# Kernel tuning notes

Hardware: AMD Instinct MI355X
Metric: run time of the kernel (lower is better)

## Reference

```python
import jax, jax.numpy as jnp
import numpy as np

N, E, H = 50000, 800000, 128
LN_EPS = 1e-5  # torch nn.LayerNorm default


def layer_norm(x, gamma, beta):
    mu = jnp.mean(x, axis=-1, keepdims=True)
    var = jnp.mean((x - mu) ** 2, axis=-1, keepdims=True)
    return (x - mu) * jax.lax.rsqrt(var + LN_EPS) * gamma + beta


def setup_inputs() -> dict:
    key = jax.random.key(0)
    ks = jax.random.split(key, 8)
    sc = 1.0 / np.sqrt(2 * H)
    return {
        "x": jax.random.normal(ks[0], (N, H), dtype=jnp.float32),
        "edge_index": jax.random.randint(ks[1], (2, E), 0, N, dtype=jnp.int64),
        "edge_weights": jax.random.uniform(ks[2], (E,), dtype=jnp.float32),
        "msg_w": jax.random.normal(ks[3], (2 * H, H), dtype=jnp.float32) * sc,
        "msg_b": jnp.zeros((H,), jnp.float32),
        "msg_g": jnp.ones((H,), jnp.float32),
        "msg_beta": jnp.zeros((H,), jnp.float32),
        "upd_w": jax.random.normal(ks[4], (2 * H, H), dtype=jnp.float32) * sc,
        "upd_b": jnp.zeros((H,), jnp.float32),
        "upd_g": jnp.ones((H,), jnp.float32),
        "upd_beta": jnp.zeros((H,), jnp.float32),
        "gate_w": jax.random.normal(ks[5], (H, 1), dtype=jnp.float32) / np.sqrt(H),
        "gate_b": jnp.zeros((1,), jnp.float32),
    }


def reference(x, edge_index, edge_weights, msg_w, msg_b, msg_g, msg_beta,
              upd_w, upd_b, upd_g, upd_beta, gate_w, gate_b):
    num_nodes = x.shape[0]
    src, dst = edge_index[0], edge_index[1]
    # per-edge gather -> MLP -> weighted message  [E, H]
    em = jnp.concatenate([x[src], x[dst]], axis=-1)          # [E, 2H]
    em = jax.nn.relu(layer_norm(em @ msg_w + msg_b, msg_g, msg_beta))
    em = em * edge_weights[:, None]
    # scatter-add to destination nodes + mean normalization
    msgs = jax.ops.segment_sum(em, dst, num_segments=num_nodes)           # [N, H]
    counts = jax.ops.segment_sum(jnp.ones((src.shape[0], 1), x.dtype), dst,
                                 num_segments=num_nodes)                  # [N, 1]
    valid = (counts > 0).astype(x.dtype)
    messages = msgs / (counts + 1e-8) * valid
    # gated update
    gate = jax.nn.sigmoid(x @ gate_w + gate_b)                            # [N, 1]
    combined = jnp.concatenate([x, messages], axis=-1)                    # [N, 2H]
    h_new = jax.nn.relu(layer_norm(combined @ upd_w + upd_b, upd_g, upd_beta))
    return gate * h_new + (1.0 - gate) * x
```

## Files before the change

### kernel.cpp

```cpp
#include <hip/hip_runtime.h>
#include <math.h>

#define H 128
#define LN_EPS 1e-5f

typedef __attribute__((ext_vector_type(8))) short  bf16x8;
typedef __attribute__((ext_vector_type(4))) float  f32x4;
typedef __attribute__((ext_vector_type(8))) unsigned short ushort8v;

__device__ __forceinline__ int imin(int a, int b) { return a < b ? a : b; }
__device__ __forceinline__ int clampi(int v, int lo, int hi) { return v < lo ? lo : (v > hi ? hi : v); }
__device__ __forceinline__ unsigned short f2bf(float f) {
    unsigned u = __float_as_uint(f);
    unsigned r = (u + 0x7fffu + ((u >> 16) & 1u)) >> 16;
    return (unsigned short)r;
}
__device__ __forceinline__ float bf2f(unsigned short u) {
    return __uint_as_float(((unsigned)u) << 16);
}

__global__ void count_kernel(const int* __restrict__ dst, int* __restrict__ cnt, int E, int n) {
    int i = blockIdx.x * blockDim.x + threadIdx.x;
    int e = i * 4;
    if (e + 3 < E) {
        int4 d4 = *(const int4*)(dst + e);
        atomicAdd(&cnt[clampi(d4.x, 0, n - 1)], 1);
        atomicAdd(&cnt[clampi(d4.y, 0, n - 1)], 1);
        atomicAdd(&cnt[clampi(d4.z, 0, n - 1)], 1);
        atomicAdd(&cnt[clampi(d4.w, 0, n - 1)], 1);
    } else {
        for (; e < E; ++e) atomicAdd(&cnt[clampi(dst[e], 0, n - 1)], 1);
    }
}

__global__ __launch_bounds__(256) void scan1_kernel(const int* __restrict__ cnt,
                                                    int* __restrict__ cursor,
                                                    int* __restrict__ bsum, int n) {
    __shared__ int wsum[4];
    const int tid = threadIdx.x, lane = tid & 63, wv = tid >> 6;
    int idx = blockIdx.x * 256 + tid;
    int v = (idx < n) ? cnt[idx] : 0;
    int s = v;
    #pragma unroll
    for (int off = 1; off < 64; off <<= 1) {
        int u = __shfl_up(s, off);
        if (lane >= off) s += u;
    }
    if (lane == 63) wsum[wv] = s;
    __syncthreads();
    int add = 0;
    for (int i = 0; i < wv; ++i) add += wsum[i];
    int incl = s + add;
    if (idx < n) cursor[idx] = incl - v;
    if (tid == 255) bsum[blockIdx.x] = incl;
}

__global__ __launch_bounds__(256) void scan2_kernel(int* __restrict__ bsum, int nb) {
    __shared__ int wsum[4];
    const int tid = threadIdx.x, lane = tid & 63, wv = tid >> 6;
    int carry = 0;
    for (int base = 0; base < nb; base += 256) {
        int idx = base + tid;
        int v = (idx < nb) ? bsum[idx] : 0;
        int s = v;
        #pragma unroll
        for (int off = 1; off < 64; off <<= 1) {
            int u = __shfl_up(s, off);
            if (lane >= off) s += u;
        }
        if (lane == 63) wsum[wv] = s;
        __syncthreads();
        int add = 0;
        for (int i = 0; i < wv; ++i) add += wsum[i];
        if (idx < nb) bsum[idx] = s + add + carry - v;
        int tot = wsum[0] + wsum[1] + wsum[2] + wsum[3];
        __syncthreads();
        carry += tot;
    }
}

__global__ void cvt_weights(const float* __restrict__ msg_w, const float* __restrict__ upd_w,
                            unsigned short* __restrict__ wtT, unsigned short* __restrict__ wbT,
                            unsigned short* __restrict__ wuT) {
    int tid = blockIdx.x * blockDim.x + threadIdx.x;
    int m = tid >> 14;
    int r = tid & 16383;
    int d = r >> 7, k = r & 127;
    float v;
    unsigned short* dstp;
    if (m == 0)      { v = msg_w[k * 128 + d];          dstp = wtT; }
    else if (m == 1) { v = msg_w[(128 + k) * 128 + d];  dstp = wbT; }
    else if (m == 2) { v = upd_w[k * 128 + d];          dstp = wuT; }
    else             { v = upd_w[(128 + k) * 128 + d];  dstp = wuT + 16384; }
    dstp[d * 128 + k] = f2bf(v);
}

__global__ __launch_bounds__(256) void pre_both_mfma(
    const float* __restrict__ x,
    const unsigned short* __restrict__ wtT, const unsigned short* __restrict__ wbT,
    const float* __restrict__ bias, unsigned short* __restrict__ xb,
    unsigned short* __restrict__ tsrcb, unsigned short* __restrict__ tdstb,
    float* __restrict__ saRow, float* __restrict__ stRow, int n,
    const int* __restrict__ src, const int* __restrict__ dst,
    const float* __restrict__ ew, int* __restrict__ cursor,
    const int* __restrict__ boff, unsigned long long* __restrict__ swP,
    int E, int epb)
{
    __shared__ unsigned short Wt[16384];
    __shared__ unsigned short Wb[16384];
    const int tid = threadIdx.x, lane = tid & 63, wv = tid >> 6;
    const int dbase = lane & 15, kgrp = lane >> 4;
    const int swzl = (dbase & 7) << 4;
    const int r0 = blockIdx.x * 64;

    const int ebase = blockIdx.x * epb;
    const int eend  = imin(ebase + epb, E);
    int hdd[4], hs[4]; float hw[4]; bool hvld[4];
    {
        #pragma unroll
        for (int u = 0; u < 4; ++u) {
            int ec = ebase + tid + u * 256;
            bool v = (ec < eend);
            int ecc = v ? ec : (E - 1);
            hdd[u] = clampi(dst[ecc], 0, n - 1);
            hs[u]  = clampi(src[ecc], 0, n - 1);
            hw[u]  = ew[ecc];
            hvld[u] = v;
        }
    }

    {
        const ushort8v* st = (const ushort8v*)wtT;
        const ushort8v* sb = (const ushort8v*)wbT;
        for (int c = tid; c < 2048; c += 256) {
            int d = c >> 4, slot = c & 15;
            int off = d * 256 + ((slot * 16) ^ ((d & 7) << 4));
            *(ushort8v*)((char*)Wt + off) = st[c];
            *(ushort8v*)((char*)Wb + off) = sb[c];
        }
    }

    int rowA = imin(r0 + wv * 16 + dbase, n - 1);
    bf16x8 a[4];
    {
        const float* xr = x + (size_t)rowA * H + kgrp * 8;
        #pragma unroll
        for (int s = 0; s < 4; ++s) {
            float4 f0 = *(const float4*)(xr + s * 32);
            float4 f1 = *(const float4*)(xr + s * 32 + 4);
            bf16x8 v;
            v[0] = (short)f2bf(f0.x); v[1] = (short)f2bf(f0.y);
            v[2] = (short)f2bf(f0.z); v[3] = (short)f2bf(f0.w);
            v[4] = (short)f2bf(f1.x); v[5] = (short)f2bf(f1.y);
            v[6] = (short)f2bf(f1.z); v[7] = (short)f2bf(f1.w);
            a[s] = v;
            *(bf16x8*)(xb + (size_t)rowA * H + s * 32 + kgrp * 8) = v;
        }
    }
    __syncthreads();

    f32x4 accT[8], accB[8];
    #pragma unroll
    for (int t = 0; t < 8; ++t) { accT[t] = (f32x4){0.f,0.f,0.f,0.f}; accB[t] = (f32x4){0.f,0.f,0.f,0.f}; }
    #pragma unroll
    for (int s = 0; s < 4; ++s) {
        #pragma unroll
        for (int t = 0; t < 8; ++t) {
            int off = (t * 16 + dbase) * 256 + ((s * 64 + kgrp * 16) ^ swzl);
            bf16x8 bt = *(const bf16x8*)((const char*)Wt + off);
            bf16x8 bb = *(const bf16x8*)((const char*)Wb + off);
            accT[t] = __builtin_amdgcn_mfma_f32_16x16x32_bf16(a[s], bt, accT[t], 0, 0, 0);
            accB[t] = __builtin_amdgcn_mfma_f32_16x16x32_bf16(a[s], bb, accB[t], 0, 0, 0);
        }
    }

    float ub[8];
    #pragma unroll
    for (int t = 0; t < 8; ++t) ub[t] = bias[t * 16 + dbase];
    #pragma unroll
    for (int r = 0; r < 4; ++r) {
        int row = r0 + wv * 16 + kgrp * 4 + r;
        if (row < n) {
            unsigned short sv[8], tv[8];
            float sa = 0.f, st = 0.f;
            #pragma unroll
            for (int t = 0; t < 8; ++t) {
                unsigned short av = f2bf(accT[t][r]);
                unsigned short dv = f2bf(accB[t][r] + ub[t]);
                sv[t] = av; tv[t] = dv;
                sa += bf2f(av); st += bf2f(dv);
            }
            #pragma unroll
            for (int t = 0; t < 8; ++t) {
                tsrcb[(size_t)row * H + t * 16 + dbase] = sv[t];
                tdstb[(size_t)row * H + t * 16 + dbase] = tv[t];
            }
            sa += __shfl_xor(sa, 1); st += __shfl_xor(st, 1);
            sa += __shfl_xor(sa, 2); st += __shfl_xor(st, 2);
            sa += __shfl_xor(sa, 4); st += __shfl_xor(st, 4);
            sa += __shfl_xor(sa, 8); st += __shfl_xor(st, 8);
            if (dbase == 0) { saRow[row] = sa; stRow[row] = st; }
        }
    }

    {
        int pp[4];
        #pragma unroll
        for (int u = 0; u < 4; ++u)
            if (hvld[u]) pp[u] = atomicAdd(&cursor[hdd[u]], 1) + boff[hdd[u] >> 8];
        #pragma unroll
        for (int u = 0; u < 4; ++u)
            if (hvld[u]) {
                unsigned long long v = ((unsigned long long)__float_as_uint(hw[u]) << 32) | (unsigned)hs[u];
                swP[pp[u]] = v;
            }
        for (int ebb = ebase + 1024; ebb < eend; ebb += 1024) {
            #pragma unroll
            for (int u = 0; u < 4; ++u) {
                int ec = ebb + tid + u * 256;
                if (ec < eend) {
                    int d = clampi(dst[ec], 0, n - 1);
                    int s = clampi(src[ec], 0, n - 1);
                    int p = atomicAdd(&cursor[d], 1) + boff[d >> 8];
                    swP[p] = ((unsigned long long)__float_as_uint(ew[ec]) << 32) | (unsigned)s;
                }
            }
        }
    }
}

__global__ __launch_bounds__(256) void node_msg_kernel(
    const unsigned short* __restrict__ tsrcb,
    const unsigned short* __restrict__ tdstb,
    const float* __restrict__ saRow, const float* __restrict__ stRow,
    const unsigned long long* __restrict__ swP,
    const int* __restrict__ cnt, const int* __restrict__ endoff,
    const int* __restrict__ boff,
    const float* __restrict__ gamma, const float* __restrict__ beta,
    unsigned short* __restrict__ msgsb, int n)
{
    const int tid  = threadIdx.x;
    const int lane = tid & 63;
    const int qq   = lane & 15;
    const int node = blockIdx.x * 16 + (tid >> 4);
    if (node >= n) return;
    const int k   = cnt[node];
    const int e0  = endoff[node] + boff[node >> 8] - k;

    float td[8];
    {
        ushort8v t = *(const ushort8v*)(tdstb + (size_t)node * H + qq * 8);
        #pragma unroll
        for (int j = 0; j < 8; ++j) td[j] = bf2f((unsigned short)t[j]);
    }
    const float St = stRow[node];
    float g_[8], b_[8];
    #pragma unroll
    for (int j = 0; j < 8; ++j) { g_[j] = gamma[qq * 8 + j]; b_[j] = beta[qq * 8 + j]; }

    float acc[8];
    #pragma unroll
    for (int j = 0; j < 8; ++j) acc[j] = 0.f;

    ushort8v A0 = {}, A1 = {};
    float W0 = 0.f, W1 = 0.f, S0 = 0.f, S1 = 0.f;
    if (k > 0) {
        unsigned long long sw = swP[e0];
        int s = (int)(unsigned)sw; W0 = __uint_as_float((unsigned)(sw >> 32));
        S0 = saRow[s]; A0 = *(const ushort8v*)(tsrcb + (size_t)s * H + qq * 8);
    }
    if (k > 1) {
        unsigned long long sw = swP[e0 + 1];
        int s = (int)(unsigned)sw; W1 = __uint_as_float((unsigned)(sw >> 32));
        S1 = saRow[s]; A1 = *(const ushort8v*)(tsrcb + (size_t)s * H + qq * 8);
    }

    for (int i = 0; i < k; i += 2) {
        ushort8v A2 = {}, A3 = {};
        float W2 = 0.f, W3 = 0.f, S2 = 0.f, S3 = 0.f;
        if (i + 2 < k) {
            unsigned long long sw = swP[e0 + i + 2];
            int s = (int)(unsigned)sw; W2 = __uint_as_float((unsigned)(sw >> 32));
            S2 = saRow[s]; A2 = *(const ushort8v*)(tsrcb + (size_t)s * H + qq * 8);
        }
        if (i + 3 < k) {
            unsigned long long sw = swP[e0 + i + 3];
            int s = (int)(unsigned)sw; W3 = __uint_as_float((unsigned)(sw >> 32));
            S3 = saRow[s]; A3 = *(const ushort8v*)(tsrcb + (size_t)s * H + qq * 8);
        }

        float v0[8], v1[8];
        float sq0 = 0.f, sq1 = 0.f;
        #pragma unroll
        for (int j = 0; j < 8; ++j) {
            v0[j] = td[j] + bf2f((unsigned short)A0[j]);
            sq0 = fmaf(v0[j], v0[j], sq0);
        }
        #pragma unroll
        for (int j = 0; j < 8; ++j) {
            v1[j] = td[j] + bf2f((unsigned short)A1[j]);
            sq1 = fmaf(v1[j], v1[j], sq1);
        }
        sq0 += __shfl_xor(sq0, 1); sq1 += __shfl_xor(sq1, 1);
        sq0 += __shfl_xor(sq0, 2); sq1 += __shfl_xor(sq1, 2);
        sq0 += __shfl_xor(sq0, 4); sq1 += __shfl_xor(sq1, 4);
        sq0 += __shfl_xor(sq0, 8); sq1 += __shfl_xor(sq1, 8);

        {
            float mu  = (S0 + St) * (1.f / 128.f);
            float var = sq0 * (1.f / 128.f) - mu * mu;
            float ri  = rsqrtf(fmaxf(var, 0.f) + LN_EPS);
            float nmr = -mu * ri;
            #pragma unroll
            for (int j = 0; j < 8; ++j) {
                float t = fmaf(v0[j], ri, nmr);
                float val = fmaf(t, g_[j], b_[j]);
                acc[j] = fmaf(fmaxf(val, 0.f), W0, acc[j]);
            }
        }
        {
            float mu  = (S1 + St) * (1.f / 128.f);
            float var = sq1 * (1.f / 128.f) - mu * mu;
            float ri  = rsqrtf(fmaxf(var, 0.f) + LN_EPS);
            float nmr = -mu * ri;
            #pragma unroll
            for (int j = 0; j < 8; ++j) {
                float t = fmaf(v1[j], ri, nmr);
                float val = fmaf(t, g_[j], b_[j]);
                acc[j] = fmaf(fmaxf(val, 0.f), W1, acc[j]);
            }
        }
        A0 = A2; W0 = W2; S0 = S2;
        A1 = A3; W1 = W3; S1 = S3;
    }

    float scale = (k > 0) ? 1.f / ((float)k + 1e-8f) : 0.f;
    ushort8v o;
    #pragma unroll
    for (int j = 0; j < 8; ++j) o[j] = f2bf(acc[j] * scale);
    *(ushort8v*)(msgsb + (size_t)node * H + qq * 8) = o;
}

__global__ __launch_bounds__(256) void update_mfma(
    const unsigned short* __restrict__ xb,
    const unsigned short* __restrict__ msgsb,
    const unsigned short* __restrict__ wuT,
    const float* __restrict__ upd_b, const float* __restrict__ g,
    const float* __restrict__ beta, const float* __restrict__ gate_w,
    const float* __restrict__ gate_b, float* __restrict__ out, int n)
{
    __shared__ unsigned short W2[2][16384];
    const int tid = threadIdx.x, lane = tid & 63, wv = tid >> 6;
    const int dbase = lane & 15, kgrp = lane >> 4;
    const int swzl = (dbase & 7) << 4;
    const int r0 = blockIdx.x * 64;

    {
        const ushort8v* srcp = (const ushort8v*)wuT;
        for (int c = tid; c < 4096; c += 256) {
            int m = c >> 11, c2 = c & 2047;
            int d = c2 >> 4, slot = c2 & 15;
            int off = m * 32768 + d * 256 + ((slot * 16) ^ ((d & 7) << 4));
            *(ushort8v*)((char*)W2 + off) = srcp[c];
        }
    }

    int rowA = imin(r0 + wv * 16 + dbase, n - 1);
    bf16x8 ax[4], am[4];
    {
        const char* arow = (const char*)(xb + (size_t)rowA * H) + kgrp * 16;
        const char* mrow = (const char*)(msgsb + (size_t)rowA * H) + kgrp * 16;
        #pragma unroll
        for (int s = 0; s < 4; ++s) {
            ax[s] = *(const bf16x8*)(arow + s * 64);
            am[s] = *(const bf16x8*)(mrow + s * 64);
        }
    }
    __syncthreads();

    f32x4 acc[8];
    #pragma unroll
    for (int t = 0; t < 8; ++t) acc[t] = (f32x4){0.f, 0.f, 0.f, 0.f};
    #pragma unroll
    for (int s = 0; s < 4; ++s) {
        #pragma unroll
        for (int t = 0; t < 8; ++t) {
            int off = (t * 16 + dbase) * 256 + ((s * 64 + kgrp * 16) ^ swzl);
            bf16x8 b = *(const bf16x8*)((const char*)W2 + off);
            acc[t] = __builtin_amdgcn_mfma_f32_16x16x32_bf16(ax[s], b, acc[t], 0, 0, 0);
        }
    }
    #pragma unroll
    for (int s = 0; s < 4; ++s) {
        #pragma unroll
        for (int t = 0; t < 8; ++t) {
            int off = 32768 + (t * 16 + dbase) * 256 + ((s * 64 + kgrp * 16) ^ swzl);
            bf16x8 b = *(const bf16x8*)((const char*)W2 + off);
            acc[t] = __builtin_amdgcn_mfma_f32_16x16x32_bf16(am[s], b, acc[t], 0, 0, 0);
        }
    }

    float ub[8], g_[8], be_[8], gw_[8];
    #pragma unroll
    for (int t = 0; t < 8; ++t) {
        int d = t * 16 + dbase;
        ub[t] = upd_b[d]; g_[t] = g[d]; be_[t] = beta[d]; gw_[t] = gate_w[d];
    }
    const float gb = gate_b[0];

    #pragma unroll
    for (int r = 0; r < 4; ++r) {
        int row = r0 + wv * 16 + kgrp * 4 + r;
        if (row >= n) continue;
        const unsigned short* xr = xb + (size_t)row * H + dbase;
        float xf[8], v[8];
        float sum = 0.f, sq = 0.f, gs = 0.f;
        #pragma unroll
        for (int t = 0; t < 8; ++t) {
            xf[t] = bf2f(xr[t * 16]);
            float val = acc[t][r] + ub[t];
            v[t] = val;
            sum += val;
            sq = fmaf(val, val, sq);
            gs = fmaf(xf[t], gw_[t], gs);
        }
        sum += __shfl_xor(sum, 1); sq += __shfl_xor(sq, 1); gs += __shfl_xor(gs, 1);
        sum += __shfl_xor(sum, 2); sq += __shfl_xor(sq, 2); gs += __shfl_xor(gs, 2);
        sum += __shfl_xor(sum, 4); sq += __shfl_xor(sq, 4); gs += __shfl_xor(gs, 4);
        sum += __shfl_xor(sum, 8); sq += __shfl_xor(sq, 8); gs += __shfl_xor(gs, 8);
        float mu  = sum * (1.f / 128.f);
        float var = sq * (1.f / 128.f) - mu * mu;
        float ri  = rsqrtf(fmaxf(var, 0.f) + LN_EPS);
        float gate = 1.f / (1.f + expf(-(gs + gb)));
        float* orow = out + (size_t)row * H + dbase;
        #pragma unroll
        for (int t = 0; t < 8; ++t) {
            float h = fmaf((v[t] - mu) * ri, g_[t], be_[t]);
            h = fmaxf(h, 0.f);
            orow[t * 16] = fmaf(gate, h - xf[t], xf[t]);
        }
    }
}

extern "C" void kernel_launch(void* const* d_in, const int* in_sizes, int n_in,
                              void* d_out, int out_size, void* d_ws, size_t ws_size,
                              hipStream_t stream)
{
    const float* x        = (const float*)d_in[0];
    const int*   ei       = (const int*)d_in[1];
    const float* ew       = (const float*)d_in[2];
    const float* msg_w    = (const float*)d_in[3];
    const float* msg_b    = (const float*)d_in[4];
    const float* msg_g    = (const float*)d_in[5];
    const float* msg_beta = (const float*)d_in[6];
    const float* upd_w    = (const float*)d_in[7];
    const float* upd_b    = (const float*)d_in[8];
    const float* upd_g    = (const float*)d_in[9];
    const float* upd_beta = (const float*)d_in[10];
    const float* gate_w   = (const float*)d_in[11];
    const float* gate_b   = (const float*)d_in[12];

    const int n = in_sizes[0] / H;
    const int E = in_sizes[2];
    const int* src = ei;
    const int* dst = ei + E;

    char* p = (char*)d_ws;
    auto alloc = [&](size_t bytes) { char* r = p; p += (bytes + 255) & ~(size_t)255; return r; };
    int*   cnt    = (int*)alloc((size_t)n * 4);
    int*   cursor = (int*)alloc((size_t)n * 4);
    int*   bsum   = (int*)alloc((size_t)1024 * 4);
    unsigned long long* swP = (unsigned long long*)alloc((size_t)E * 8);
    float* saRow  = (float*)alloc((size_t)n * 4);
    float* stRow  = (float*)alloc((size_t)n * 4);
    unsigned short* xb    = (unsigned short*)alloc((size_t)n * H * 2);
    unsigned short* tsrcb = (unsigned short*)alloc((size_t)n * H * 2);
    unsigned short* tdstb = (unsigned short*)alloc((size_t)n * H * 2);
    unsigned short* msgsb = (unsigned short*)alloc((size_t)n * H * 2);
    unsigned short* wtT   = (unsigned short*)alloc((size_t)H * H * 2);
    unsigned short* wbT   = (unsigned short*)alloc((size_t)H * H * 2);
    unsigned short* wuT   = (unsigned short*)alloc((size_t)2 * H * H * 2);

    hipMemsetAsync(cnt, 0, (size_t)n * 4, stream);

    const int nb = (n + 255) / 256;
    int eb4 = ((E + 3) / 4 + 255) / 256;
    count_kernel<<<eb4, 256, 0, stream>>>(dst, cnt, E, n);
    scan1_kernel<<<nb, 256, 0, stream>>>(cnt, cursor, bsum, n);
    scan2_kernel<<<1, 256, 0, stream>>>(bsum, nb);

    cvt_weights<<<256, 256, 0, stream>>>(msg_w, upd_w, wtT, wbT, wuT);

    const int nblocks = (n + 63) / 64;
    const int epb = (E + nblocks - 1) / nblocks;
    pre_both_mfma<<<nblocks, 256, 0, stream>>>(x, wtT, wbT, msg_b, xb, tsrcb, tdstb,
                                               saRow, stRow, n,
                                               src, dst, ew, cursor, bsum, swP, E, epb);

    node_msg_kernel<<<(n + 15) / 16, 256, 0, stream>>>(tsrcb, tdstb, saRow, stRow, swP,
                                                       cnt, cursor, bsum,
                                                       msg_g, msg_beta, msgsb, n);

    update_mfma<<<(n + 63) / 64, 256, 0, stream>>>(xb, msgsb, wuT, upd_b, upd_g, upd_beta,
                                                   gate_w, gate_b, (float*)d_out, n);
}
```

Measured before the change: 187.8 us.

## Assign one wavefront per node, splitting its edges across four lane groups

The per-node message kernel now maps a whole 64-lane wavefront to each node instead of a 16-lane group. The four 16-lane groups each take every fourth incoming edge, and their partial sums are combined with cross-lane shuffles before one group writes the result. The aim is to spread high-degree nodes' serial edge loops across more lanes and cut latency per node. In exchange it launches four times as many blocks, leaves lanes idle on low-degree nodes, and drops the two-edge software prefetch in favour of a one-ahead prefetch per group.

```diff
diff --git a/kernel.cpp b/kernel.cpp
--- a/kernel.cpp
+++ b/kernel.cpp
@@ -241,8 +241,9 @@
 {
     const int tid  = threadIdx.x;
     const int lane = tid & 63;
+    const int grp  = lane >> 4;
     const int qq   = lane & 15;
-    const int node = blockIdx.x * 16 + (tid >> 4);
+    const int node = blockIdx.x * 4 + (tid >> 6);
     if (node >= n) return;
     const int k   = cnt[node];
     const int e0  = endoff[node] + boff[node >> 8] - k;
@@ -262,83 +263,61 @@
     #pragma unroll
     for (int j = 0; j < 8; ++j) acc[j] = 0.f;
 
-    ushort8v A0 = {}, A1 = {};
-    float W0 = 0.f, W1 = 0.f, S0 = 0.f, S1 = 0.f;
-    if (k > 0) {
-        unsigned long long sw = swP[e0];
+    ushort8v A0 = {};
+    float W0 = 0.f, S0 = 0.f;
+    if (grp < k) {
+        unsigned long long sw = swP[e0 + grp];
         int s = (int)(unsigned)sw; W0 = __uint_as_float((unsigned)(sw >> 32));
         S0 = saRow[s]; A0 = *(const ushort8v*)(tsrcb + (size_t)s * H + qq * 8);
     }
-    if (k > 1) {
-        unsigned long long sw = swP[e0 + 1];
-        int s = (int)(unsigned)sw; W1 = __uint_as_float((unsigned)(sw >> 32));
-        S1 = saRow[s]; A1 = *(const ushort8v*)(tsrcb + (size_t)s * H + qq * 8);
-    }
-
-    for (int i = 0; i < k; i += 2) {
-        ushort8v A2 = {}, A3 = {};
-        float W2 = 0.f, W3 = 0.f, S2 = 0.f, S3 = 0.f;
-        if (i + 2 < k) {
-            unsigned long long sw = swP[e0 + i + 2];
-            int s = (int)(unsigned)sw; W2 = __uint_as_float((unsigned)(sw >> 32));
-            S2 = saRow[s]; A2 = *(const ushort8v*)(tsrcb + (size_t)s * H + qq * 8);
-        }
-        if (i + 3 < k) {
-            unsigned long long sw = swP[e0 + i + 3];
-            int s = (int)(unsigned)sw; W3 = __uint_as_float((unsigned)(sw >> 32));
-            S3 = saRow[s]; A3 = *(const ushort8v*)(tsrcb + (size_t)s * H + qq * 8);
-        }
-
-        float v0[8], v1[8];
-        float sq0 = 0.f, sq1 = 0.f;
+
+    for (int i = 0; i < k; i += 4) {
+        ushort8v A1 = {};
+        float W1 = 0.f, S1 = 0.f;
+        int jn = i + 4 + grp;
+        if (jn < k) {
+            unsigned long long sw = swP[e0 + jn];
+            int s = (int)(unsigned)sw; W1 = __uint_as_float((unsigned)(sw >> 32));
+            S1 = saRow[s]; A1 = *(const ushort8v*)(tsrcb + (size_t)s * H + qq * 8);
+        }
+
+        float v[8], sq = 0.f;
         #pragma unroll
         for (int j = 0; j < 8; ++j) {
-            v0[j] = td[j] + bf2f((unsigned short)A0[j]);
-            sq0 = fmaf(v0[j], v0[j], sq0);
-        }
+            v[j] = td[j] + bf2f((unsigned short)A0[j]);
+            sq = fmaf(v[j], v[j], sq);
+        }
+        sq += __shfl_xor(sq, 1);
+        sq += __shfl_xor(sq, 2);
+        sq += __shfl_xor(sq, 4);
+        sq += __shfl_xor(sq, 8);
+
+        float mu  = (S0 + St) * (1.f / 128.f);
+        float var = sq * (1.f / 128.f) - mu * mu;
+        float ri  = rsqrtf(fmaxf(var, 0.f) + LN_EPS);
+        float nmr = -mu * ri;
         #pragma unroll
         for (int j = 0; j < 8; ++j) {
-            v1[j] = td[j] + bf2f((unsigned short)A1[j]);
-            sq1 = fmaf(v1[j], v1[j], sq1);
-        }
-        sq0 += __shfl_xor(sq0, 1); sq1 += __shfl_xor(sq1, 1);
-        sq0 += __shfl_xor(sq0, 2); sq1 += __shfl_xor(sq1, 2);
-        sq0 += __shfl_xor(sq0, 4); sq1 += __shfl_xor(sq1, 4);
-        sq0 += __shfl_xor(sq0, 8); sq1 += __shfl_xor(sq1, 8);
-
-        {
-            float mu  = (S0 + St) * (1.f / 128.f);
-            float var = sq0 * (1.f / 128.f) - mu * mu;
-            float ri  = rsqrtf(fmaxf(var, 0.f) + LN_EPS);
-            float nmr = -mu * ri;
-            #pragma unroll
-            for (int j = 0; j < 8; ++j) {
-                float t = fmaf(v0[j], ri, nmr);
-                float val = fmaf(t, g_[j], b_[j]);
-                acc[j] = fmaf(fmaxf(val, 0.f), W0, acc[j]);
-            }
-        }
-        {
-            float mu  = (S1 + St) * (1.f / 128.f);
-            float var = sq1 * (1.f / 128.f) - mu * mu;
-            float ri  = rsqrtf(fmaxf(var, 0.f) + LN_EPS);
-            float nmr = -mu * ri;
-            #pragma unroll
-            for (int j = 0; j < 8; ++j) {
-                float t = fmaf(v1[j], ri, nmr);
-                float val = fmaf(t, g_[j], b_[j]);
-                acc[j] = fmaf(fmaxf(val, 0.f), W1, acc[j]);
-            }
-        }
-        A0 = A2; W0 = W2; S0 = S2;
-        A1 = A3; W1 = W3; S1 = S3;
-    }
-
-    float scale = (k > 0) ? 1.f / ((float)k + 1e-8f) : 0.f;
-    ushort8v o;
-    #pragma unroll
-    for (int j = 0; j < 8; ++j) o[j] = f2bf(acc[j] * scale);
-    *(ushort8v*)(msgsb + (size_t)node * H + qq * 8) = o;
+            float t = fmaf(v[j], ri, nmr);
+            float val = fmaf(t, g_[j], b_[j]);
+            acc[j] = fmaf(fmaxf(val, 0.f), W0, acc[j]);
+        }
+        A0 = A1; W0 = W1; S0 = S1;
+    }
+
+    #pragma unroll
+    for (int j = 0; j < 8; ++j) {
+        acc[j] += __shfl_xor(acc[j], 16);
+        acc[j] += __shfl_xor(acc[j], 32);
+    }
+
+    if (grp == 0) {
+        float scale = (k > 0) ? 1.f / ((float)k + 1e-8f) : 0.f;
+        ushort8v o;
+        #pragma unroll
+        for (int j = 0; j < 8; ++j) o[j] = f2bf(acc[j] * scale);
+        *(ushort8v*)(msgsb + (size_t)node * H + qq * 8) = o;
+    }
 }
 
 __global__ __launch_bounds__(256) void update_mfma(
@@ -497,9 +476,9 @@
                                                saRow, stRow, n,
                                                src, dst, ew, cursor, bsum, swP, E, epb);
 
-    node_msg_kernel<<<(n + 15) / 16, 256, 0, stream>>>(tsrcb, tdstb, saRow, stRow, swP,
-                                                       cnt, cursor, bsum,
-                                                       msg_g, msg_beta, msgsb, n);
+    node_msg_kernel<<<(n + 3) / 4, 256, 0, stream>>>(tsrcb, tdstb, saRow, stRow, swP,
+                                                     cnt, cursor, bsum,
+                                                     msg_g, msg_beta, msgsb, n);
 
     update_mfma<<<(n + 63) / 64, 256, 0, stream>>>(xb, msgsb, wuT, upd_b, upd_g, upd_beta,
                                                    gate_w, gate_b, (float*)d_out, n);
```

New measurement: 176.4 us. 6.1% less time.
